# Kernel tuning notes

Hardware: AMD Instinct MI355X
Metric: run time of the kernel (lower is better)

Reference implementation:

```python
import jax, jax.numpy as jnp
import numpy as np

T_DAYS, IN_DIM, H = 50000, 12, 512
PIN, POUT, OUT_DIM = 27, 3, 2
# physical_forward scale factors applied to the column means
SCALES = np.array([400,1,1,1,1,12,10,10,1,1,1,1,1,10,1,1,1,5,1,1,4,1,1,180,1,1,10], np.float32)
# last-layer bias of parnet chosen so constrained params land near published PRELES defaults
BIAS27 = np.array([1.03,0.45,0.118,3.0,0.748,1.1,0.05,1.85,-0.18,0.035,-0.2007,0.5,-0.364,
                   0.0324,0.874,0.07,0.8473,0.12,1.2,0.33,1.0,0.0,0.0,1.1,0.0,0.0,2.0], np.float32)

def _elu(v):
    return jnp.where(v > 0, v, jnp.expm1(v))

def _constrain(p):
    # faithful jax port of parameter_constraint (clamp/relu/sigmoid per column)
    sig = jax.nn.sigmoid
    cols = [jnp.clip(p[:,0],0,2), jax.nn.relu(p[:,1]), jax.nn.relu(p[:,2]), p[:,3],
            jnp.clip(p[:,4],0,2.5), jnp.clip(p[:,5],0.01,3), jnp.clip(p[:,6],-0.2,2.1),
            jnp.clip(p[:,7],0.23,3.0), jnp.clip(p[:,8],-1,0), jnp.clip(p[:,9],0,0.7),
            sig(p[:,10]), p[:,11], p[:,12], jnp.clip(p[:,13],0,1.0), jnp.clip(p[:,14],0,1.2),
            jnp.clip(p[:,15],0,2.5), sig(p[:,16]), jnp.clip(p[:,17],0,1), p[:,18],
            jnp.clip(p[:,19],0,1/0.75), jax.nn.relu(p[:,20]), jax.nn.relu(p[:,21]), p[:,22],
            jax.nn.relu(p[:,23]), jax.nn.relu(p[:,24]), jax.nn.relu(p[:,25]), jax.nn.relu(p[:,26])]
    return jnp.stack(cols, axis=1)

def _preles(pm, cin):
    # PRELES daily LUE model (etmodel=0, LOGFLAG=0, t0=-999 so fPheno=1), run as one lax.scan
    (soildepth, ThetaFC, ThetaPWP, tauDrainage, beta, tau, S0, Smax, kappa, gamma,
     soilthres, bCO2, xCO2, ETbeta, ETkappa, ETchi, ETsoilthres, ETnu, MeltCoef,
     I0, CWmax, SnowThreshold, T0, SWinit, CWinit, SOGinit, Sinit) = [pm[i] for i in range(27)]
    fcap = ThetaFC * soildepth

    def step(carry, day):
        S, theta, snow, canw = carry
        precip, tair, par, vpd, fapar, co2 = day[0], day[1], day[2], day[3], day[4], day[6]
        # temperature acclimation state and fS
        S = S + (tair - S) / tau
        fS = jnp.minimum(jnp.maximum(S - S0, 0.0) / Smax, 1.0)
        # GPP modifiers
        thetavol = theta / soildepth
        REW = (thetavol - ThetaPWP) / (ThetaFC - ThetaPWP)
        fD = jnp.minimum(jnp.exp(kappa * vpd), 1.0)
        fW = jnp.where(REW < soilthres, jnp.where(REW > 0.01, REW / soilthres, 0.0), 1.0)
        fL = 1.0 / (gamma * par + 1.0)
        fE = jnp.minimum(fD, fW)
        gpp380 = beta * par * fapar * fS * fL * fE
        gpp = gpp380 * (1.0 + bCO2 * jnp.log(co2 / 380.0))
        # interception + canopy water store
        intercepted = jnp.where(tair > SnowThreshold, precip * I0 * fapar / 0.75, 0.0)
        rain = precip - intercepted
        cap = CWmax * fapar
        over = intercepted + canw > cap
        small_cw = CWmax <= 1e-8
        tf = jnp.where(small_cw, rain + intercepted,
                       jnp.where(over, rain + intercepted + canw - cap, rain))
        canw = jnp.where(small_cw, canw, jnp.where(over, cap, canw + intercepted))
        # snow pack (degree-day melt)
        newsnow = jnp.where(tair < SnowThreshold, tf, 0.0)
        tf = tf - newsnow
        melt = jnp.where(tair >= T0, MeltCoef * (tair - T0), 0.0)
        melt = jnp.minimum(melt, snow + newsnow)
        snow = snow + newsnow - melt
        # evapotranspiration, etmodel = 0
        fWet = jnp.where(REW < ETsoilthres, jnp.where(REW > 0.01, REW / ETsoilthres, 0.0), 1.0)
        fWet = jnp.where(canw > 1e-8, 1.0, fWet)
        fCO2et = 1.0 + xCO2 * jnp.log(co2 / 380.0)
        transp = vpd * ETbeta * gpp380 / jnp.power(vpd, ETkappa) * jnp.power(jnp.maximum(fW, 1e-12), ETnu) * fCO2et
        evap = ETchi * (1.0 - fapar) * fWet * par
        et = transp + evap
        # soil water balance: evaporate wet canopy then snow, rest from soil
        canw2 = jnp.maximum(canw - et, 0.0)
        rem = jnp.maximum(et - canw, 0.0)
        snow2 = jnp.maximum(snow - rem, 0.0)
        etsoil = jnp.maximum(rem - snow, 0.0)
        st0 = jnp.maximum(theta + tf + melt - etsoil, 1e-4)
        drain = jnp.where(tauDrainage > 0, jnp.maximum(st0 - fcap, 0.0) / tauDrainage, 0.0)
        theta = st0 - drain
        return (S, theta, snow2, canw2), (gpp, et, theta)

    init = (Sinit, SWinit, SOGinit, CWinit)
    _, (GPP, ET, SWout) = jax.lax.scan(step, init, cin)
    return GPP, ET, SWout

def setup_inputs():
    key = jax.random.key(0)
    ks = jax.random.split(key, 12)
    x = jax.random.normal(ks[0], (T_DAYS, IN_DIM), jnp.float32)
    u = jax.random.uniform(ks[1], (T_DAYS, 7), jnp.float32)
    tn = jax.random.normal(ks[2], (T_DAYS,), jnp.float32)
    doy = (jnp.arange(T_DAYS) % 365 + 1).astype(jnp.float32)
    seas = jnp.sin(2 * jnp.pi * (doy - 120) / 365.0)
    precip = jnp.where(u[:, 0] > 0.7, u[:, 0] * 20.0, 0.0)        # mm/day
    tair = 5.0 + 12.0 * seas + 3.0 * tn                            # degC
    par = jnp.maximum(10.0 + 8.0 * seas + 3.0 * jax.random.normal(ks[3], (T_DAYS,), jnp.float32), 0.1)
    vpd = 0.1 + 2.0 * u[:, 3]                                      # kPa, kept > 0.1
    fapar = 0.3 + 0.5 * u[:, 4]
    co2 = 380.0 + 40.0 * u[:, 6]                                   # ppm
    cin = jnp.stack([precip, tair, par, vpd, fapar, doy, co2], axis=1)
    def lin(k, fi, fo, scale, bias=None):
        w = jax.random.normal(k, (fi, fo), jnp.float32) * scale
        b = jnp.zeros((fo,), jnp.float32) if bias is None else jnp.asarray(bias)
        return w, b
    pW0, pb0 = lin(ks[4], IN_DIM, H, 1.0 / np.sqrt(IN_DIM))
    pW1, pb1 = lin(ks[5], H, H, 1.0 / np.sqrt(H))
    pW2, pb2 = lin(ks[6], H, PIN, 0.01, BIAS27)
    rW0, rb0 = lin(ks[7], POUT, H, 1.0 / np.sqrt(POUT))
    rW1, rb1 = lin(ks[8], H, H, 1.0 / np.sqrt(H))
    rW2, rb2 = lin(ks[9], H, OUT_DIM, 1.0 / np.sqrt(H))
    sw = jnp.array([150.0, 50.0], jnp.float32)
    return dict(x=x, cin=cin, sw=sw, tp=1,
                pW0=pW0, pb0=pb0, pW1=pW1, pb1=pb1, pW2=pW2, pb2=pb2,
                rW0=rW0, rb0=rb0, rW1=rW1, rb1=rb1, rW2=rW2, rb2=rb2)

def reference(x, cin, sw, tp, pW0, pb0, pW1, pb1, pW2, pb2, rW0, rb0, rW1, rb1, rW2, rb2):
    # parnet: Linear -> ELU -> Linear -> Linear (single ELU due to add_module name reuse)
    h = _elu(x @ pW0 + pb0)
    h = h @ pW1 + pb1
    praw = h @ pW2 + pb2                      # [T, 27]
    p = _constrain(praw)
    pm = p.mean(axis=0) * jnp.asarray(SCALES)  # per-parameter mean, physical scaling
    GPP, ET, SW = _preles(pm, cin)
    ppreds = jnp.stack([GPP, ET, (SW - sw[0]) / sw[1]], axis=1)  # tp is not None path
    # resnet: Linear -> ELU -> Linear -> Linear
    g = _elu(ppreds @ rW0 + rb0)
    g = g @ rW1 + rb1
    y_hat = g @ rW2 + rb2
    return y_hat, ppreds
```

## Files before the change

### kernel.cpp

```cpp
#include <hip/hip_runtime.h>
#include <hip/hip_bf16.h>

#define T_DAYS   50000
#define HDIM     512
#define NP       27
#define NROWBLK  196

#define NCHUNK   1024
#define CHUNK_L  49
#define WARM     256
#define ITERS    (WARM + CHUNK_L)
#define GRP      8
#define NG       40
#define DPAD     50688
#define DBLK     198

static_assert(NG*GRP >= ITERS, "scan must cover all iterations");
static_assert((NG & 1) == 0, "NG must be even for the ping-pong");
static_assert(1023*CHUNK_L + (NG+1)*GRP - 1 < DPAD, "prefetch stays in padded records");

#define OFF_PJ    0
#define OFF_PR0   20480
#define OFF_RW12  22528
#define OFF_B12   23552
#define OFF_RB12  23579
#define OFF_PART  23584
#define OFF_PM    28880
#define OFF_DA    29184
#define OFF_DB    (OFF_DA + DPAD*4)
#define OFF_DC    (OFF_DB + DPAD*4)
#define OFF_PPT   (OFF_DC + DPAD)
#define WS_FAST_FLOATS (OFF_PPT + CHUNK_L*NCHUNK*3)
#define WS_FAST_BYTES  ((size_t)WS_FAST_FLOATS * 4)

typedef float f32x4 __attribute__((ext_vector_type(4)));

__constant__ float c_SCALES[NP] = {400,1,1,1,1,12,10,10,1,1,1,1,1,10,1,1,1,5,1,1,4,1,1,180,1,1,10};

__device__ __forceinline__ float sane(float v, float lo, float hi) {
  v = (v == v) ? v : 0.f;
  return fminf(fmaxf(v, lo), hi);
}

__device__ __forceinline__ void ldg4(f32x4& d, const f32x4* p) {
  asm volatile("global_load_dwordx4 %0, %1, off" : "=v"(d) : "v"(p));
}
__device__ __forceinline__ void ldg1(float& d, const float* p) {
  asm volatile("global_load_dword %0, %1, off" : "=v"(d) : "v"(p));
}
__device__ __forceinline__ void wait_vm0() {
  asm volatile("s_waitcnt vmcnt(0)" ::: "memory");
  __builtin_amdgcn_sched_barrier(0);
}

__global__ void k_prep(const float* pW0, const float* pb0, const float* pW1,
                       const float* pb1, const float* pW2, const float* pb2,
                       const float* rW0, const float* rb0, const float* rW1,
                       const float* rb1, const float* rW2, const float* rb2,
                       float* ws) {
  __shared__ __align__(16) float col[HDIM];
  const int bid = blockIdx.x, tid = threadIdx.x;
  if (bid < NP) {
    for (int k = tid; k < HDIM; k += 256) col[k] = pW2[k*NP + bid];
    __syncthreads();
    const float4* c4 = (const float4*)col;
    for (int i = tid; i < HDIM; i += 256) {
      const float4* wrow = (const float4*)(pW1 + i*HDIM);
      float acc = 0.f;
      #pragma unroll 4
      for (int k = 0; k < HDIM/4; ++k) {
        float4 w = wrow[k], cv = c4[k];
        acc += w.x*cv.x + w.y*cv.y + w.z*cv.z + w.w*cv.w;
      }
      ws[OFF_PJ + i*40 + 12 + bid] = acc;
    }
    if (tid == 0) {
      float acc = 0.f;
      for (int k = 0; k < HDIM; ++k) acc += pb1[k] * col[k];
      ws[OFF_B12 + bid] = acc + pb2[bid];
    }
  } else if (bid < NP + 2) {
    const int j2 = bid - NP;
    for (int k = tid; k < HDIM; k += 256) col[k] = rW2[k*2 + j2];
    __syncthreads();
    const float4* c4 = (const float4*)col;
    for (int i = tid; i < HDIM; i += 256) {
      const float4* wrow = (const float4*)(rW1 + i*HDIM);
      float acc = 0.f;
      #pragma unroll 4
      for (int k = 0; k < HDIM/4; ++k) {
        float4 w = wrow[k], cv = c4[k];
        acc += w.x*cv.x + w.y*cv.y + w.z*cv.z + w.w*cv.w;
      }
      ws[OFF_RW12 + i*2 + j2] = acc;
    }
    if (tid == 0) {
      float acc = 0.f;
      for (int k = 0; k < HDIM; ++k) acc += rb1[k] * col[k];
      ws[OFF_RB12 + j2] = acc + rb2[j2];
    }
  } else {
    for (int j = tid; j < HDIM; j += 256) {
      for (int k = 0; k < 12; ++k) ws[OFF_PJ + j*40 + k] = pW0[k*HDIM + j];
      ws[OFF_PJ + j*40 + 39] = pb0[j];
      float4 v;
      v.x = rW0[0*HDIM + j]; v.y = rW0[1*HDIM + j];
      v.z = rW0[2*HDIM + j]; v.w = rb0[j];
      ((float4*)(ws + OFF_PR0))[j] = v;
    }
  }
}

__global__ void __launch_bounds__(256) k_parnet(const float* x, float* ws) {
  __shared__ float4 spj[256*10];
  const int t = blockIdx.x*256 + threadIdx.x;

  float xr[12];
  if (t < T_DAYS) {
    const float4* xp = (const float4*)(x + t*12);
    float4 x0 = xp[0], x1 = xp[1], x2 = xp[2];
    xr[0]=x0.x; xr[1]=x0.y; xr[2]=x0.z; xr[3]=x0.w;
    xr[4]=x1.x; xr[5]=x1.y; xr[6]=x1.z; xr[7]=x1.w;
    xr[8]=x2.x; xr[9]=x2.y; xr[10]=x2.z; xr[11]=x2.w;
  } else {
    #pragma unroll
    for (int k = 0; k < 12; ++k) xr[k] = 0.f;
  }

  float acc[NP];
  #pragma unroll
  for (int c = 0; c < NP; ++c) acc[c] = ws[OFF_B12 + c];

  for (int half = 0; half < 2; ++half) {
    __syncthreads();
    const float4* src = ((const float4*)(ws + OFF_PJ)) + half*2560;
    for (int idx = threadIdx.x; idx < 2560; idx += 256) spj[idx] = src[idx];
    __syncthreads();
    for (int j = 0; j < 256; ++j) {
      const float4* row = &spj[j*10];
      float4 a = row[0], b = row[1], cc = row[2];
      float wf[28];
      #pragma unroll
      for (int q = 0; q < 7; ++q) {
        float4 v = row[3 + q];
        wf[4*q] = v.x; wf[4*q+1] = v.y; wf[4*q+2] = v.z; wf[4*q+3] = v.w;
      }
      float h = a.x*xr[0] + a.y*xr[1] + a.z*xr[2] + a.w*xr[3]
              + b.x*xr[4] + b.y*xr[5] + b.z*xr[6] + b.w*xr[7]
              + cc.x*xr[8] + cc.y*xr[9] + cc.z*xr[10] + cc.w*xr[11]
              + wf[27];
      h = h > 0.f ? h : (__expf(h) - 1.f);
      #pragma unroll
      for (int c = 0; c < NP; ++c) acc[c] += h * wf[c];
    }
  }

  auto clip = [] (float v, float lo, float hi) { return fminf(fmaxf(v, lo), hi); };
  acc[0]  = clip(acc[0], 0.f, 2.f);
  acc[1]  = fmaxf(acc[1], 0.f);
  acc[2]  = fmaxf(acc[2], 0.f);
  acc[4]  = clip(acc[4], 0.f, 2.5f);
  acc[5]  = clip(acc[5], 0.01f, 3.f);
  acc[6]  = clip(acc[6], -0.2f, 2.1f);
  acc[7]  = clip(acc[7], 0.23f, 3.0f);
  acc[8]  = clip(acc[8], -1.f, 0.f);
  acc[9]  = clip(acc[9], 0.f, 0.7f);
  acc[10] = 1.f/(1.f + __expf(-acc[10]));
  acc[13] = clip(acc[13], 0.f, 1.0f);
  acc[14] = clip(acc[14], 0.f, 1.2f);
  acc[15] = clip(acc[15], 0.f, 2.5f);
  acc[16] = 1.f/(1.f + __expf(-acc[16]));
  acc[17] = clip(acc[17], 0.f, 1.f);
  acc[19] = clip(acc[19], 0.f, (float)(1.0/0.75));
  acc[20] = fmaxf(acc[20], 0.f);
  acc[21] = fmaxf(acc[21], 0.f);
  acc[23] = fmaxf(acc[23], 0.f);
  acc[24] = fmaxf(acc[24], 0.f);
  acc[25] = fmaxf(acc[25], 0.f);
  acc[26] = fmaxf(acc[26], 0.f);
  if (t >= T_DAYS) {
    #pragma unroll
    for (int c = 0; c < NP; ++c) acc[c] = 0.f;
  }

  #pragma unroll
  for (int c = 0; c < NP; ++c) {
    float v = acc[c];
    #pragma unroll
    for (int off = 32; off >= 1; off >>= 1) v += __shfl_down(v, off, 64);
    acc[c] = v;
  }
  __shared__ float red[4][NP];
  const int wv = threadIdx.x >> 6, ln = threadIdx.x & 63;
  if (ln == 0) {
    #pragma unroll
    for (int c = 0; c < NP; ++c) red[wv][c] = acc[c];
  }
  __syncthreads();
  if (threadIdx.x < NP) {
    float s = red[0][threadIdx.x] + red[1][threadIdx.x] + red[2][threadIdx.x] + red[3][threadIdx.x];
    ws[OFF_PART + blockIdx.x*NP + threadIdx.x] = s;
  }
}

__global__ void k_finalize(float* ws) {
  const int c = threadIdx.x;
  if (c < NP) {
    float s = 0.f;
    for (int b = 0; b < NROWBLK; ++b) s += ws[OFF_PART + b*NP + c];
    ws[OFF_PM + c] = sane(s * (1.f/(float)T_DAYS) * c_SCALES[c], -1e6f, 1e6f);
  }
}

__global__ void __launch_bounds__(256) k_days(const float* ws_in, const float* cin, float* ws) {
  const int tp = blockIdx.x*256 + threadIdx.x;
  if (tp >= DPAD) return;
  const float* pm = ws_in + OFF_PM;
  const float beta = pm[4], kappa = pm[8], gamma = pm[9], bCO2 = pm[11], xCO2 = pm[12];
  const float ETbeta = pm[13], ETkappa = pm[14], ETchi = pm[15], MeltCoef = pm[18];
  const float I0 = pm[19], CWmax = pm[20], SnowThr = pm[21], T0 = pm[22];

  int t = tp - WARM;
  t = t < 0 ? 0 : (t >= T_DAYS ? T_DAYS - 1 : t);
  const float precip = sane(cin[t*7+0], 0.f, 1e4f);
  const float tair   = sane(cin[t*7+1], -150.f, 150.f);
  const float par    = sane(cin[t*7+2], 0.f, 1e4f);
  const float vpd    = sane(cin[t*7+3], 1e-3f, 1e3f);
  const float fapar  = sane(cin[t*7+4], 0.f, 1.f);
  const float co2    = sane(cin[t*7+6], 1.f, 1e5f);

  const float logc = __logf(co2 * (1.f/380.f));
  const float fD   = fminf(__expf(kappa*vpd), 1.f);
  const float G    = beta * par * fapar * (1.f/(gamma*par + 1.f));
  const float Cc   = 1.f + bCO2*logc;
  const float Bq   = ETbeta * __powf(vpd, 1.f - ETkappa) * (1.f + xCO2*logc);
  const float E    = ETchi * (1.f - fapar) * par;
  const float icpt = (tair > SnowThr) ? precip*I0*fapar*(1.f/0.75f) : 0.f;
  const float rain = precip - icpt;
  const float cap  = CWmax * fapar;
  const float mpot = (tair >= T0) ? MeltCoef*(tair - T0) : 0.f;

  ((float4*)(ws + OFF_DA))[tp] = make_float4(fD, G*Cc, Bq*G, E);
  ((float4*)(ws + OFF_DB))[tp] = make_float4(rain, cap, icpt, mpot);
  ws[OFF_DC + tp] = tair;
}

__global__ void __launch_bounds__(64, 1) k_scan_fast(float* ws, const float* sw) {
  const int lane = threadIdx.x;
  const int c = blockIdx.x*64 + lane;
  const float* pm = ws + OFF_PM;
  const float soildepth = pm[0], ThetaFC = pm[1], ThetaPWP = pm[2];
  const float tauD = pm[3], tau = pm[5], S0 = pm[6], Smax = pm[7];
  const float soilthres = pm[10], ETsoilthres = pm[16], ETnu = pm[17];
  const float SnowThr = pm[21];
  const float SWinit = pm[23], CWinit = pm[24], SOGinit = pm[25], Sinit = pm[26];
  const float CWmax = pm[20];

  float dFC = ThetaFC - ThetaPWP; if (!(fabsf(dFC) > 1e-12f)) dFC = 1e-12f;
  float sd  = soildepth;          if (!(fabsf(sd)  > 1e-12f)) sd  = 1e-12f;

  const float invtau = 1.f/fmaxf(tau, 1e-6f), invSmax = 1.f/fmaxf(Smax, 1e-12f);
  const float rc1 = 1.f/(sd*dFC);
  const float rc0 = -ThetaPWP/dFC;
  const float inv_st = 1.f/fmaxf(soilthres, 1e-30f);
  const float inv_est = 1.f/fmaxf(ETsoilthres, 1e-30f);
  const float fcap = ThetaFC*soildepth;
  const float invtauD = (tauD > 0.f) ? 1.f/tauD : 0.f;
  const bool small_cw = (CWmax <= 1e-8f);
  const float sw0 = sane(sw[0], -1e6f, 1e6f);
  const float sw1v = sw[1];
  const float invsw1 = 1.f/((fabsf(sw1v) > 1e-12f) ? sw1v : 1e-12f);

  float S = Sinit, theta = SWinit, snow = SOGinit, canw = CWinit;
  const int i_lo = (c*CHUNK_L < WARM) ? (WARM - c*CHUNK_L) : 0;

  const f32x4* gA = ((const f32x4*)(ws + OFF_DA)) + c*CHUNK_L;
  const f32x4* gB = ((const f32x4*)(ws + OFF_DB)) + c*CHUNK_L;
  const float* gC = (ws + OFF_DC) + c*CHUNK_L;
  float* ppt = ws + OFF_PPT;

  auto step = [&](const f32x4 dA, const f32x4 dB, const float tairv, const int i,
                  float& o0, float& o1, float& o2) {
    if (i < i_lo) return;
    const float fD = dA.x, GC = dA.y, BG = dA.z, E = dA.w;
    const float rain = dB.x, cap = dB.y, icpt = dB.z, mpot = dB.w;

    S += (tairv - S)*invtau;
    S = fminf(fmaxf(S, -1e4f), 1e4f);
    const float fS = fminf(fmaxf(S - S0, 0.f)*invSmax, 1.f);

    const float REW = theta*rc1 + rc0;
    float fW   = (REW >= soilthres)   ? 1.f : ((REW > 0.01f) ? REW*inv_st  : 0.f);
    float fWet = (REW >= ETsoilthres) ? 1.f : ((REW > 0.01f) ? REW*inv_est : 0.f);

    const float precip = rain + icpt;
    const bool over = (icpt + canw > cap);
    const float tf  = small_cw ? precip : (over ? precip + canw - cap : rain);
    const float cw  = small_cw ? canw   : (over ? cap : canw + icpt);
    if (cw > 1e-8f) fWet = 1.f;

    const bool cold = (tairv < SnowThr);
    const float newsnow = cold ? tf : 0.f;
    const float tf2     = cold ? 0.f : tf;
    const float sn = snow + newsnow;
    const float snow_mid = fmaxf(sn - mpot, 0.f);
    const float melt = sn - snow_mid;

    const float sfe = fS * fminf(fD, fW);
    float pw = 1.f;
    if (fW < 1.f) pw = __powf(fmaxf(fW, 1e-12f), ETnu);
    const float transp = BG*sfe*pw;
    const float evap = E*fWet;
    const float et = transp + evap;

    canw = fminf(fmaxf(cw - et, 0.f), 1e4f);
    const float rem = fmaxf(et - cw, 0.f);
    snow = fminf(fmaxf(snow_mid - rem, 0.f), 1e6f);
    const float etsoil = fmaxf(rem - snow_mid, 0.f);
    const float st0 = fmaxf(theta + tf2 + melt - etsoil, 1e-4f);
    const float dr = fmaxf(st0 - fcap, 0.f)*invtauD;
    theta = fminf(fmaxf(st0 - dr, 1e-4f), 1e6f);

    o0 = sane(GC*sfe, -1e6f, 1e6f);
    o1 = sane(et, -1e6f, 1e6f);
    o2 = sane((theta - sw0)*invsw1, -1e6f, 1e6f);
  };

  f32x4 A0[GRP], B0[GRP]; float C0[GRP];
  f32x4 A1[GRP], B1[GRP]; float C1[GRP];
  float poA[GRP*3], poB[GRP*3];

#define ISSUE(GG, A, B, C) do { \
  _Pragma("unroll") for (int k = 0; k < GRP; ++k) { \
    const int ii = (GG)*GRP + k; \
    ldg4(A[k], gA + ii); ldg4(B[k], gB + ii); ldg1(C[k], gC + ii); \
  } __builtin_amdgcn_sched_barrier(0); } while (0)

#define COMPUTE(GG, A, B, C, PO) do { \
  _Pragma("unroll") for (int k = 0; k < GRP; ++k) \
    step(A[k], B[k], C[k], (GG)*GRP + k, PO[k*3], PO[k*3+1], PO[k*3+2]); \
  __builtin_amdgcn_sched_barrier(0); } while (0)

#define FLUSH(GF, PO) do { \
  _Pragma("unroll") for (int k = 0; k < GRP; ++k) { \
    const int io = (GF)*GRP + k - WARM; \
    if (io >= 0 && io < CHUNK_L) { \
      float* pp = ppt + (io*NCHUNK + c)*3; \
      pp[0] = PO[k*3]; pp[1] = PO[k*3+1]; pp[2] = PO[k*3+2]; \
    } } } while (0)

  ISSUE(0, A0, B0, C0);
  for (int g = 0; g < NG; g += 2) {
    wait_vm0();
    ISSUE(g + 1, A1, B1, C1);
    if (g > 0) FLUSH(g - 1, poB);
    COMPUTE(g, A0, B0, C0, poA);

    wait_vm0();
    ISSUE(g + 2, A0, B0, C0);
    FLUSH(g, poA);
    COMPUTE(g + 1, A1, B1, C1, poB);
  }
  FLUSH(NG - 1, poB);

#undef ISSUE
#undef COMPUTE
#undef FLUSH
}

__global__ void __launch_bounds__(256) k_resnet_fast(const float* ws, float* out) {
  __shared__ float4 spr[HDIM];
  __shared__ float2 srw[HDIM];
  for (int idx = threadIdx.x; idx < HDIM; idx += 256) {
    spr[idx] = ((const float4*)(ws + OFF_PR0))[idx];
    srw[idx] = ((const float2*)(ws + OFF_RW12))[idx];
  }
  __syncthreads();
  const int t = blockIdx.x*256 + threadIdx.x;
  if (t >= T_DAYS) return;
  const int c = t / CHUNK_L, i = t - c*CHUNK_L;
  const int r = (i*NCHUNK + c)*3;
  const float p0 = ws[OFF_PPT + r + 0];
  const float p1 = ws[OFF_PPT + r + 1];
  const float p2 = ws[OFF_PPT + r + 2];
  float y0 = ws[OFF_RB12], y1 = ws[OFF_RB12 + 1];
  for (int j = 0; j < HDIM; ++j) {
    const float4 a = spr[j];
    float g = p0*a.x + p1*a.y + p2*a.z + a.w;
    g = g > 0.f ? g : (__expf(g) - 1.f);
    const float2 r2 = srw[j];
    y0 += g*r2.x; y1 += g*r2.y;
  }
  out[t*2 + 0] = sane(y0, -1e6f, 1e6f);
  out[t*2 + 1] = sane(y1, -1e6f, 1e6f);
  out[2*T_DAYS + t*3 + 0] = p0;
  out[2*T_DAYS + t*3 + 1] = p1;
  out[2*T_DAYS + t*3 + 2] = p2;
}

struct DayR { float fD, G, Cc, Bq, E, rain, cap, icpt, mpot, tair; };

__device__ __forceinline__ DayR mkday(const float* cin, int t,
    float beta, float kappa, float gamma, float bCO2, float xCO2, float ETbeta,
    float ETkappa, float ETchi, float MeltCoef, float I0, float CWmax,
    float SnowThr, float T0) {
  int tt = t < 0 ? 0 : (t >= T_DAYS ? T_DAYS - 1 : t);
  const float precip = sane(cin[tt*7+0], 0.f, 1e4f);
  const float tair   = sane(cin[tt*7+1], -150.f, 150.f);
  const float par    = sane(cin[tt*7+2], 0.f, 1e4f);
  const float vpd    = sane(cin[tt*7+3], 1e-3f, 1e3f);
  const float fapar  = sane(cin[tt*7+4], 0.f, 1.f);
  const float co2    = sane(cin[tt*7+6], 1.f, 1e5f);
  const float logc = __logf(co2 * (1.f/380.f));
  DayR d;
  d.fD   = fminf(__expf(kappa*vpd), 1.f);
  d.G    = beta * par * fapar * (1.f/(gamma*par + 1.f));
  d.Cc   = 1.f + bCO2*logc;
  d.Bq   = ETbeta * __powf(vpd, 1.f - ETkappa) * (1.f + xCO2*logc);
  d.E    = ETchi * (1.f - fapar) * par;
  d.icpt = (tair > SnowThr) ? precip*I0*fapar*(1.f/0.75f) : 0.f;
  d.rain = precip - d.icpt;
  d.cap  = CWmax * fapar;
  d.mpot = (tair >= T0) ? MeltCoef*(tair - T0) : 0.f;
  d.tair = tair;
  return d;
}

__global__ void __launch_bounds__(64) k_scan_slow(const float* ws, const float* cin,
                                                 const float* sw, float* out) {
  const int c = blockIdx.x*64 + threadIdx.x;
  const float* pm = ws + OFF_PM;
  const float soildepth = pm[0], ThetaFC = pm[1], ThetaPWP = pm[2];
  const float tauD = pm[3], beta = pm[4], tau = pm[5], S0 = pm[6], Smax = pm[7];
  const float kappa = pm[8], gamma = pm[9], soilthres = pm[10], bCO2 = pm[11];
  const float xCO2 = pm[12], ETbeta = pm[13], ETkappa = pm[14], ETchi = pm[15];
  const float ETsoilthres = pm[16], ETnu = pm[17], MeltCoef = pm[18], I0 = pm[19];
  const float CWmax = pm[20], SnowThr = pm[21], T0 = pm[22];
  const float SWinit = pm[23], CWinit = pm[24], SOGinit = pm[25], Sinit = pm[26];

  float dFC = ThetaFC - ThetaPWP; if (!(fabsf(dFC) > 1e-12f)) dFC = 1e-12f;
  float sd  = soildepth;          if (!(fabsf(sd)  > 1e-12f)) sd  = 1e-12f;

  const float invtau = 1.f/fmaxf(tau, 1e-6f), invSmax = 1.f/fmaxf(Smax, 1e-12f);
  const float rc1 = 1.f/(sd*dFC);
  const float rc0 = -ThetaPWP/dFC;
  const float inv_st = 1.f/fmaxf(soilthres, 1e-30f);
  const float inv_est = 1.f/fmaxf(ETsoilthres, 1e-30f);
  const float fcap = ThetaFC*soildepth;
  const float invtauD = (tauD > 0.f) ? 1.f/tauD : 0.f;
  const bool small_cw = (CWmax <= 1e-8f);
  const float sw0 = sane(sw[0], -1e6f, 1e6f);
  const float sw1v = sw[1];
  const float invsw1 = 1.f/((fabsf(sw1v) > 1e-12f) ? sw1v : 1e-12f);

  float S = Sinit, theta = SWinit, snow = SOGinit, canw = CWinit;
  const int s  = c*CHUNK_L - WARM;
  const int e0 = c*CHUNK_L;

  DayR dA = mkday(cin, s,   beta,kappa,gamma,bCO2,xCO2,ETbeta,ETkappa,ETchi,MeltCoef,I0,CWmax,SnowThr,T0);
  DayR dB = mkday(cin, s+1, beta,kappa,gamma,bCO2,xCO2,ETbeta,ETkappa,ETchi,MeltCoef,I0,CWmax,SnowThr,T0);

  for (int i = 0; i < ITERS; ++i) {
    const DayR d = dA;
    dA = dB;
    dB = mkday(cin, s + i + 2, beta,kappa,gamma,bCO2,xCO2,ETbeta,ETkappa,ETchi,MeltCoef,I0,CWmax,SnowThr,T0);

    const int t = s + i;
    if (t >= 0 && t < T_DAYS) {
      S += (d.tair - S)*invtau;
      S = fminf(fmaxf(S, -1e4f), 1e4f);
      const float fS = fminf(fmaxf(S - S0, 0.f)*invSmax, 1.f);

      const float REW = theta*rc1 + rc0;
      float fW   = (REW >= soilthres)   ? 1.f : ((REW > 0.01f) ? REW*inv_st  : 0.f);
      float fWet = (REW >= ETsoilthres) ? 1.f : ((REW > 0.01f) ? REW*inv_est : 0.f);

      const float precip = d.rain + d.icpt;
      const bool over = (d.icpt + canw > d.cap);
      const float tf  = small_cw ? precip : (over ? precip + canw - d.cap : d.rain);
      const float cw  = small_cw ? canw   : (over ? d.cap : canw + d.icpt);
      if (cw > 1e-8f) fWet = 1.f;

      const bool cold = (d.tair < SnowThr);
      const float newsnow = cold ? tf : 0.f;
      const float tf2     = cold ? 0.f : tf;
      const float sn = snow + newsnow;
      const float snow_mid = fmaxf(sn - d.mpot, 0.f);
      const float melt = sn - snow_mid;

      const float fE = fminf(d.fD, fW);
      const float gpp380 = d.G*fS*fE;
      float pw = 1.f;
      if (fW < 1.f) pw = __powf(fmaxf(fW, 1e-12f), ETnu);
      const float transp = d.Bq*gpp380*pw;
      const float evap = d.E*fWet;
      const float et = transp + evap;

      canw = fminf(fmaxf(cw - et, 0.f), 1e4f);
      const float rem = fmaxf(et - cw, 0.f);
      snow = fminf(fmaxf(snow_mid - rem, 0.f), 1e6f);
      const float etsoil = fmaxf(rem - snow_mid, 0.f);
      const float st0 = fmaxf(theta + tf2 + melt - etsoil, 1e-4f);
      const float dr = fmaxf(st0 - fcap, 0.f)*invtauD;
      theta = fminf(fmaxf(st0 - dr, 1e-4f), 1e6f);

      if (t >= e0) {
        out[2*T_DAYS + t*3 + 0] = sane(gpp380*d.Cc, -1e6f, 1e6f);
        out[2*T_DAYS + t*3 + 1] = sane(et, -1e6f, 1e6f);
        out[2*T_DAYS + t*3 + 2] = sane((theta - sw0)*invsw1, -1e6f, 1e6f);
      }
    }
  }
}

__global__ void __launch_bounds__(256) k_resnet_slow(const float* ws, float* out) {
  const int t = blockIdx.x*256 + threadIdx.x;
  if (t >= T_DAYS) return;
  const float p0 = out[2*T_DAYS + t*3 + 0];
  const float p1 = out[2*T_DAYS + t*3 + 1];
  const float p2 = out[2*T_DAYS + t*3 + 2];
  const float4* pr = (const float4*)(ws + OFF_PR0);
  const float2* rw = (const float2*)(ws + OFF_RW12);
  float y0 = ws[OFF_RB12], y1 = ws[OFF_RB12 + 1];
  for (int j = 0; j < HDIM; ++j) {
    const float4 a = pr[j];
    float g = p0*a.x + p1*a.y + p2*a.z + a.w;
    g = g > 0.f ? g : (__expf(g) - 1.f);
    const float2 r = rw[j];
    y0 += g*r.x; y1 += g*r.y;
  }
  out[t*2 + 0] = sane(y0, -1e6f, 1e6f);
  out[t*2 + 1] = sane(y1, -1e6f, 1e6f);
}

extern "C" void kernel_launch(void* const* d_in, const int* in_sizes, int n_in,
                              void* d_out, int out_size, void* d_ws, size_t ws_size,
                              hipStream_t stream) {
  const float* x   = (const float*)d_in[0];
  const float* cin = (const float*)d_in[1];
  const float* sw  = (const float*)d_in[2];
  const float *pW0 = (const float*)d_in[4],  *pb0 = (const float*)d_in[5];
  const float *pW1 = (const float*)d_in[6],  *pb1 = (const float*)d_in[7];
  const float *pW2 = (const float*)d_in[8],  *pb2 = (const float*)d_in[9];
  const float *rW0 = (const float*)d_in[10], *rb0 = (const float*)d_in[11];
  const float *rW1 = (const float*)d_in[12], *rb1 = (const float*)d_in[13];
  const float *rW2 = (const float*)d_in[14], *rb2 = (const float*)d_in[15];
  float* ws  = (float*)d_ws;
  float* out = (float*)d_out;

  k_prep<<<dim3(NP+3), dim3(256), 0, stream>>>(pW0,pb0,pW1,pb1,pW2,pb2,rW0,rb0,rW1,rb1,rW2,rb2, ws);
  k_parnet<<<dim3(NROWBLK), dim3(256), 0, stream>>>(x, ws);
  k_finalize<<<dim3(1), dim3(32), 0, stream>>>(ws);

  if (ws_size >= WS_FAST_BYTES) {
    k_days<<<dim3(DBLK), dim3(256), 0, stream>>>(ws, cin, ws);
    k_scan_fast<<<dim3(NCHUNK/64), dim3(64), 0, stream>>>(ws, sw);
    k_resnet_fast<<<dim3(NROWBLK), dim3(256), 0, stream>>>(ws, out);
  } else {
    k_scan_slow<<<dim3(NCHUNK/64), dim3(64), 0, stream>>>(ws, cin, sw, out);
    k_resnet_slow<<<dim3(NROWBLK), dim3(256), 0, stream>>>(ws, out);
  }
}
```

Before: 299.5 us.

## Split hidden-dim across warps in parnet/resnet and double scan chunk count

The parnet and resnet kernels now use 512-thread blocks covering 128 days each, splitting the 512 hidden units into four slices that are reduced through shared memory. This raises block count and parallelism on a GPU that was underfilled with 196 blocks. The chunked scan doubles NCHUNK to 2048 with shorter chunks, so more parallel lanes share the same warm-up length. The finalize reduction is spread over 256 threads, and the prep dot products use four independent accumulators. The trade-off is extra shared-memory reduction traffic and more warm-up work in the scan relative to useful days.

```diff
diff --git a/kernel.cpp b/kernel.cpp
--- a/kernel.cpp
+++ b/kernel.cpp
@@ -5,19 +5,20 @@
 #define HDIM     512
 #define NP       27
 #define NROWBLK  196
-
-#define NCHUNK   1024
-#define CHUNK_L  49
+#define NBLK2    391
+
+#define NCHUNK   2048
+#define CHUNK_L  25
 #define WARM     256
 #define ITERS    (WARM + CHUNK_L)
 #define GRP      8
-#define NG       40
-#define DPAD     50688
-#define DBLK     198
+#define NG       36
+#define DPAD     51712
+#define DBLK     202
 
 static_assert(NG*GRP >= ITERS, "scan must cover all iterations");
 static_assert((NG & 1) == 0, "NG must be even for the ping-pong");
-static_assert(1023*CHUNK_L + (NG+1)*GRP - 1 < DPAD, "prefetch stays in padded records");
+static_assert((NCHUNK-1)*CHUNK_L + (NG+1)*GRP - 1 < DPAD, "prefetch stays in padded records");
 
 #define OFF_PJ    0
 #define OFF_PR0   20480
@@ -25,8 +26,8 @@
 #define OFF_B12   23552
 #define OFF_RB12  23579
 #define OFF_PART  23584
-#define OFF_PM    28880
-#define OFF_DA    29184
+#define OFF_PM    34144
+#define OFF_DA    34176
 #define OFF_DB    (OFF_DA + DPAD*4)
 #define OFF_DC    (OFF_DB + DPAD*4)
 #define OFF_PPT   (OFF_DC + DPAD)
@@ -66,13 +67,13 @@
     const float4* c4 = (const float4*)col;
     for (int i = tid; i < HDIM; i += 256) {
       const float4* wrow = (const float4*)(pW1 + i*HDIM);
-      float acc = 0.f;
+      float a0 = 0.f, a1 = 0.f, a2 = 0.f, a3 = 0.f;
       #pragma unroll 4
       for (int k = 0; k < HDIM/4; ++k) {
         float4 w = wrow[k], cv = c4[k];
-        acc += w.x*cv.x + w.y*cv.y + w.z*cv.z + w.w*cv.w;
+        a0 += w.x*cv.x; a1 += w.y*cv.y; a2 += w.z*cv.z; a3 += w.w*cv.w;
       }
-      ws[OFF_PJ + i*40 + 12 + bid] = acc;
+      ws[OFF_PJ + i*40 + 12 + bid] = (a0 + a1) + (a2 + a3);
     }
     if (tid == 0) {
       float acc = 0.f;
@@ -86,13 +87,13 @@
     const float4* c4 = (const float4*)col;
     for (int i = tid; i < HDIM; i += 256) {
       const float4* wrow = (const float4*)(rW1 + i*HDIM);
-      float acc = 0.f;
+      float a0 = 0.f, a1 = 0.f, a2 = 0.f, a3 = 0.f;
       #pragma unroll 4
       for (int k = 0; k < HDIM/4; ++k) {
         float4 w = wrow[k], cv = c4[k];
-        acc += w.x*cv.x + w.y*cv.y + w.z*cv.z + w.w*cv.w;
+        a0 += w.x*cv.x; a1 += w.y*cv.y; a2 += w.z*cv.z; a3 += w.w*cv.w;
       }
-      ws[OFF_RW12 + i*2 + j2] = acc;
+      ws[OFF_RW12 + i*2 + j2] = (a0 + a1) + (a2 + a3);
     }
     if (tid == 0) {
       float acc = 0.f;
@@ -111,9 +112,12 @@
   }
 }
 
-__global__ void __launch_bounds__(256) k_parnet(const float* x, float* ws) {
+__global__ void __launch_bounds__(512) k_parnet(const float* x, float* ws) {
   __shared__ float4 spj[256*10];
-  const int t = blockIdx.x*256 + threadIdx.x;
+  __shared__ float red[2][NP];
+  const int tid = threadIdx.x;
+  const int d = tid & 127, s = tid >> 7;
+  const int t = blockIdx.x*128 + d;
 
   float xr[12];
   if (t < T_DAYS) {
@@ -129,86 +133,111 @@
 
   float acc[NP];
   #pragma unroll
-  for (int c = 0; c < NP; ++c) acc[c] = ws[OFF_B12 + c];
+  for (int c = 0; c < NP; ++c) acc[c] = (s == 0) ? ws[OFF_B12 + c] : 0.f;
 
   for (int half = 0; half < 2; ++half) {
     __syncthreads();
     const float4* src = ((const float4*)(ws + OFF_PJ)) + half*2560;
-    for (int idx = threadIdx.x; idx < 2560; idx += 256) spj[idx] = src[idx];
+    for (int idx = tid; idx < 2560; idx += 512) spj[idx] = src[idx];
     __syncthreads();
-    for (int j = 0; j < 256; ++j) {
-      const float4* row = &spj[j*10];
-      float4 a = row[0], b = row[1], cc = row[2];
-      float wf[28];
+    const float4* base = &spj[(s*64)*10];
+    for (int j = 0; j < 64; ++j) {
+      const float4* r = base + j*10;
+      float h = r[0].x*xr[0] + r[0].y*xr[1] + r[0].z*xr[2] + r[0].w*xr[3]
+              + r[1].x*xr[4] + r[1].y*xr[5] + r[1].z*xr[6] + r[1].w*xr[7]
+              + r[2].x*xr[8] + r[2].y*xr[9] + r[2].z*xr[10] + r[2].w*xr[11]
+              + r[9].w;
+      h = h > 0.f ? h : (__expf(h) - 1.f);
       #pragma unroll
       for (int q = 0; q < 7; ++q) {
-        float4 v = row[3 + q];
-        wf[4*q] = v.x; wf[4*q+1] = v.y; wf[4*q+2] = v.z; wf[4*q+3] = v.w;
+        const float4 v = r[3 + q];
+        if (4*q + 0 < NP) acc[4*q + 0] += h * v.x;
+        if (4*q + 1 < NP) acc[4*q + 1] += h * v.y;
+        if (4*q + 2 < NP) acc[4*q + 2] += h * v.z;
+        if (4*q + 3 < NP) acc[4*q + 3] += h * v.w;
       }
-      float h = a.x*xr[0] + a.y*xr[1] + a.z*xr[2] + a.w*xr[3]
-              + b.x*xr[4] + b.y*xr[5] + b.z*xr[6] + b.w*xr[7]
-              + cc.x*xr[8] + cc.y*xr[9] + cc.z*xr[10] + cc.w*xr[11]
-              + wf[27];
-      h = h > 0.f ? h : (__expf(h) - 1.f);
+    }
+  }
+
+  float* scratch = (float*)spj;
+  __syncthreads();
+  if (s >= 2) {
+    #pragma unroll
+    for (int c = 0; c < NP; ++c) scratch[((s-2)*128 + d)*NP + c] = acc[c];
+  }
+  __syncthreads();
+  if (s < 2) {
+    #pragma unroll
+    for (int c = 0; c < NP; ++c) acc[c] += scratch[(s*128 + d)*NP + c];
+  }
+  __syncthreads();
+  if (s == 1) {
+    #pragma unroll
+    for (int c = 0; c < NP; ++c) scratch[d*NP + c] = acc[c];
+  }
+  __syncthreads();
+  if (s == 0) {
+    #pragma unroll
+    for (int c = 0; c < NP; ++c) acc[c] += scratch[d*NP + c];
+
+    auto clip = [] (float v, float lo, float hi) { return fminf(fmaxf(v, lo), hi); };
+    acc[0]  = clip(acc[0], 0.f, 2.f);
+    acc[1]  = fmaxf(acc[1], 0.f);
+    acc[2]  = fmaxf(acc[2], 0.f);
+    acc[4]  = clip(acc[4], 0.f, 2.5f);
+    acc[5]  = clip(acc[5], 0.01f, 3.f);
+    acc[6]  = clip(acc[6], -0.2f, 2.1f);
+    acc[7]  = clip(acc[7], 0.23f, 3.0f);
+    acc[8]  = clip(acc[8], -1.f, 0.f);
+    acc[9]  = clip(acc[9], 0.f, 0.7f);
+    acc[10] = 1.f/(1.f + __expf(-acc[10]));
+    acc[13] = clip(acc[13], 0.f, 1.0f);
+    acc[14] = clip(acc[14], 0.f, 1.2f);
+    acc[15] = clip(acc[15], 0.f, 2.5f);
+    acc[16] = 1.f/(1.f + __expf(-acc[16]));
+    acc[17] = clip(acc[17], 0.f, 1.f);
+    acc[19] = clip(acc[19], 0.f, (float)(1.0/0.75));
+    acc[20] = fmaxf(acc[20], 0.f);
+    acc[21] = fmaxf(acc[21], 0.f);
+    acc[23] = fmaxf(acc[23], 0.f);
+    acc[24] = fmaxf(acc[24], 0.f);
+    acc[25] = fmaxf(acc[25], 0.f);
+    acc[26] = fmaxf(acc[26], 0.f);
+    if (t >= T_DAYS) {
       #pragma unroll
-      for (int c = 0; c < NP; ++c) acc[c] += h * wf[c];
-    }
-  }
-
-  auto clip = [] (float v, float lo, float hi) { return fminf(fmaxf(v, lo), hi); };
-  acc[0]  = clip(acc[0], 0.f, 2.f);
-  acc[1]  = fmaxf(acc[1], 0.f);
-  acc[2]  = fmaxf(acc[2], 0.f);
-  acc[4]  = clip(acc[4], 0.f, 2.5f);
-  acc[5]  = clip(acc[5], 0.01f, 3.f);
-  acc[6]  = clip(acc[6], -0.2f, 2.1f);
-  acc[7]  = clip(acc[7], 0.23f, 3.0f);
-  acc[8]  = clip(acc[8], -1.f, 0.f);
-  acc[9]  = clip(acc[9], 0.f, 0.7f);
-  acc[10] = 1.f/(1.f + __expf(-acc[10]));
-  acc[13] = clip(acc[13], 0.f, 1.0f);
-  acc[14] = clip(acc[14], 0.f, 1.2f);
-  acc[15] = clip(acc[15], 0.f, 2.5f);
-  acc[16] = 1.f/(1.f + __expf(-acc[16]));
-  acc[17] = clip(acc[17], 0.f, 1.f);
-  acc[19] = clip(acc[19], 0.f, (float)(1.0/0.75));
-  acc[20] = fmaxf(acc[20], 0.f);
-  acc[21] = fmaxf(acc[21], 0.f);
-  acc[23] = fmaxf(acc[23], 0.f);
-  acc[24] = fmaxf(acc[24], 0.f);
-  acc[25] = fmaxf(acc[25], 0.f);
-  acc[26] = fmaxf(acc[26], 0.f);
-  if (t >= T_DAYS) {
+      for (int c = 0; c < NP; ++c) acc[c] = 0.f;
+    }
     #pragma unroll
-    for (int c = 0; c < NP; ++c) acc[c] = 0.f;
-  }
-
-  #pragma unroll
-  for (int c = 0; c < NP; ++c) {
-    float v = acc[c];
+    for (int c = 0; c < NP; ++c) {
+      float v = acc[c];
+      #pragma unroll
+      for (int off = 32; off >= 1; off >>= 1) v += __shfl_down(v, off, 64);
+      acc[c] = v;
+    }
+    if ((tid & 63) == 0) {
+      #pragma unroll
+      for (int c = 0; c < NP; ++c) red[tid >> 6][c] = acc[c];
+    }
+  }
+  __syncthreads();
+  if (tid < NP) ws[OFF_PART + blockIdx.x*NP + tid] = red[0][tid] + red[1][tid];
+}
+
+__global__ void __launch_bounds__(256) k_finalize(float* ws) {
+  const int tid = threadIdx.x;
+  const int c = tid >> 3, s = tid & 7;
+  float p = 0.f;
+  if (c < NP) {
+    for (int b = s; b < NBLK2; b += 8) p += ws[OFF_PART + b*NP + c];
+  }
+  __shared__ float fr[32][8];
+  if (c < 32) fr[c][s] = p;
+  __syncthreads();
+  if (tid < NP) {
+    float q = 0.f;
     #pragma unroll
-    for (int off = 32; off >= 1; off >>= 1) v += __shfl_down(v, off, 64);
-    acc[c] = v;
-  }
-  __shared__ float red[4][NP];
-  const int wv = threadIdx.x >> 6, ln = threadIdx.x & 63;
-  if (ln == 0) {
-    #pragma unroll
-    for (int c = 0; c < NP; ++c) red[wv][c] = acc[c];
-  }
-  __syncthreads();
-  if (threadIdx.x < NP) {
-    float s = red[0][threadIdx.x] + red[1][threadIdx.x] + red[2][threadIdx.x] + red[3][threadIdx.x];
-    ws[OFF_PART + blockIdx.x*NP + threadIdx.x] = s;
-  }
-}
-
-__global__ void k_finalize(float* ws) {
-  const int c = threadIdx.x;
-  if (c < NP) {
-    float s = 0.f;
-    for (int b = 0; b < NROWBLK; ++b) s += ws[OFF_PART + b*NP + c];
-    ws[OFF_PM + c] = sane(s * (1.f/(float)T_DAYS) * c_SCALES[c], -1e6f, 1e6f);
+    for (int k = 0; k < 8; ++k) q += fr[tid][k];
+    ws[OFF_PM + tid] = sane(q * (1.f/(float)T_DAYS) * c_SCALES[tid], -1e6f, 1e6f);
   }
 }
 
@@ -368,34 +397,44 @@
 #undef FLUSH
 }
 
-__global__ void __launch_bounds__(256) k_resnet_fast(const float* ws, float* out) {
+__global__ void __launch_bounds__(512) k_resnet_fast(const float* ws, float* out) {
   __shared__ float4 spr[HDIM];
   __shared__ float2 srw[HDIM];
-  for (int idx = threadIdx.x; idx < HDIM; idx += 256) {
+  __shared__ float sy0[512], sy1[512];
+  const int tid = threadIdx.x;
+  for (int idx = tid; idx < HDIM; idx += 512) {
     spr[idx] = ((const float4*)(ws + OFF_PR0))[idx];
     srw[idx] = ((const float2*)(ws + OFF_RW12))[idx];
   }
-  __syncthreads();
-  const int t = blockIdx.x*256 + threadIdx.x;
-  if (t >= T_DAYS) return;
-  const int c = t / CHUNK_L, i = t - c*CHUNK_L;
+  const int d = tid & 127, s = tid >> 7;
+  const int t = blockIdx.x*128 + d;
+  const int tc = t < T_DAYS ? t : T_DAYS - 1;
+  const int c = tc / CHUNK_L, i = tc - c*CHUNK_L;
   const int r = (i*NCHUNK + c)*3;
+  __syncthreads();
   const float p0 = ws[OFF_PPT + r + 0];
   const float p1 = ws[OFF_PPT + r + 1];
   const float p2 = ws[OFF_PPT + r + 2];
-  float y0 = ws[OFF_RB12], y1 = ws[OFF_RB12 + 1];
-  for (int j = 0; j < HDIM; ++j) {
+  float y0 = (s == 0) ? ws[OFF_RB12]     : 0.f;
+  float y1 = (s == 0) ? ws[OFF_RB12 + 1] : 0.f;
+  for (int j = s*128; j < s*128 + 128; ++j) {
     const float4 a = spr[j];
     float g = p0*a.x + p1*a.y + p2*a.z + a.w;
     g = g > 0.f ? g : (__expf(g) - 1.f);
     const float2 r2 = srw[j];
     y0 += g*r2.x; y1 += g*r2.y;
   }
-  out[t*2 + 0] = sane(y0, -1e6f, 1e6f);
-  out[t*2 + 1] = sane(y1, -1e6f, 1e6f);
-  out[2*T_DAYS + t*3 + 0] = p0;
-  out[2*T_DAYS + t*3 + 1] = p1;
-  out[2*T_DAYS + t*3 + 2] = p2;
+  sy0[tid] = y0; sy1[tid] = y1;
+  __syncthreads();
+  if (s == 0 && t < T_DAYS) {
+    y0 = (sy0[d] + sy0[128 + d]) + (sy0[256 + d] + sy0[384 + d]);
+    y1 = (sy1[d] + sy1[128 + d]) + (sy1[256 + d] + sy1[384 + d]);
+    out[t*2 + 0] = sane(y0, -1e6f, 1e6f);
+    out[t*2 + 1] = sane(y1, -1e6f, 1e6f);
+    out[2*T_DAYS + t*3 + 0] = p0;
+    out[2*T_DAYS + t*3 + 1] = p1;
+    out[2*T_DAYS + t*3 + 2] = p2;
+  }
 }
 
 struct DayR { float fD, G, Cc, Bq, E, rain, cap, icpt, mpot, tair; };
@@ -549,13 +588,13 @@
   float* out = (float*)d_out;
 
   k_prep<<<dim3(NP+3), dim3(256), 0, stream>>>(pW0,pb0,pW1,pb1,pW2,pb2,rW0,rb0,rW1,rb1,rW2,rb2, ws);
-  k_parnet<<<dim3(NROWBLK), dim3(256), 0, stream>>>(x, ws);
-  k_finalize<<<dim3(1), dim3(32), 0, stream>>>(ws);
+  k_parnet<<<dim3(NBLK2), dim3(512), 0, stream>>>(x, ws);
+  k_finalize<<<dim3(1), dim3(256), 0, stream>>>(ws);
 
   if (ws_size >= WS_FAST_BYTES) {
     k_days<<<dim3(DBLK), dim3(256), 0, stream>>>(ws, cin, ws);
     k_scan_fast<<<dim3(NCHUNK/64), dim3(64), 0, stream>>>(ws, sw);
-    k_resnet_fast<<<dim3(NROWBLK), dim3(256), 0, stream>>>(ws, out);
+    k_resnet_fast<<<dim3(NBLK2), dim3(512), 0, stream>>>(ws, out);
   } else {
     k_scan_slow<<<dim3(NCHUNK/64), dim3(64), 0, stream>>>(ws, cin, sw, out);
     k_resnet_slow<<<dim3(NROWBLK), dim3(256), 0, stream>>>(ws, out);
```

Result: faster. 292.7 us (-2.3%).
